# Kernel tuning notes

Measured on AMD Instinct MI355X. Metric: run time of the kernel, lower is better.

## Reference

```python
import jax, jax.numpy as jnp
import numpy as np

N_NODES = 50000
N_EDGES = 800000
IN_CH = 128
HID = 128
OUT_CH = 10
N_GRAPHS = 64
BN_EPS = 1e-5


def _lin_init(k, fan_in, fan_out):
    k1, k2 = jax.random.split(k)
    s = 1.0 / np.sqrt(fan_in)
    W = jax.random.uniform(k1, (fan_in, fan_out), minval=-s, maxval=s, dtype=jnp.float32)
    b = jax.random.uniform(k2, (fan_out,), minval=-s, maxval=s, dtype=jnp.float32)
    return W, b


def setup_inputs() -> dict:
    key = jax.random.key(0)
    ks = jax.random.split(key, 12)
    x = jax.random.normal(ks[0], (N_NODES, IN_CH), dtype=jnp.float32)
    edge_index = jax.random.randint(ks[1], (2, N_EDGES), 0, N_NODES, dtype=jnp.int32)
    batch = jnp.sort(jax.random.randint(ks[2], (N_NODES,), 0, N_GRAPHS, dtype=jnp.int32))
    Wb0, bb0 = _lin_init(ks[3], IN_CH, HID)
    Wb1, bb1 = _lin_init(ks[4], HID, HID)
    Wa0, ba0 = _lin_init(ks[5], HID, HID)
    Wa1, ba1 = _lin_init(ks[6], HID, HID)
    Wa2, ba2 = _lin_init(ks[7], HID, HID)
    Wh0, bh0 = _lin_init(ks[8], HID, HID)
    Wh1, bh1 = _lin_init(ks[9], HID, HID)
    Wh2, bh2 = _lin_init(ks[10], HID, OUT_CH)
    ones = jnp.ones((HID,), jnp.float32)
    zeros = jnp.zeros((HID,), jnp.float32)
    return {
        'x': x, 'edge_index': edge_index, 'batch': batch, 'num_graphs': N_GRAPHS,
        'Wb0': Wb0, 'bb0': bb0, 'gb0': ones, 'betab0': zeros, 'Wb1': Wb1, 'bb1': bb1,
        'Wa0': Wa0, 'ba0': ba0, 'ga0': ones, 'bea0': zeros,
        'Wa1': Wa1, 'ba1': ba1, 'ga1': ones, 'bea1': zeros,
        'Wa2': Wa2, 'ba2': ba2,
        'Wh0': Wh0, 'bh0': bh0, 'Wh1': Wh1, 'bh1': bh1, 'Wh2': Wh2, 'bh2': bh2,
    }


def _gcn_edges(edge_index, n):
    # add self-loops, symmetric deg^{-1/2} normalization (PyG GCNConv default)
    loop = jnp.arange(n, dtype=edge_index.dtype)
    src = jnp.concatenate([edge_index[0], loop])
    dst = jnp.concatenate([edge_index[1], loop])
    deg = jax.ops.segment_sum(jnp.ones_like(dst, dtype=jnp.float32), dst, num_segments=n)
    dinv = jnp.where(deg > 0, jax.lax.rsqrt(deg), 0.0)
    return src, dst, dinv[src] * dinv[dst]


def _conv(h, W, b, src, dst, ew, n):
    hw = h @ W  # [N, F_out]
    agg = jax.ops.segment_sum(hw[src] * ew[:, None], dst, num_segments=n)
    return agg + b


def _bn(h, g, b):
    # BatchNorm1d with track_running_stats=False -> always batch statistics
    mean = jnp.mean(h, axis=0)
    var = jnp.var(h, axis=0)
    return g * (h - mean) * jax.lax.rsqrt(var + BN_EPS) + b


def _gelu(h):
    return jax.nn.gelu(h, approximate=False)


def reference(x, edge_index, batch, num_graphs,
              Wb0, bb0, gb0, betab0, Wb1, bb1,
              Wa0, ba0, ga0, bea0, Wa1, ba1, ga1, bea1, Wa2, ba2,
              Wh0, bh0, Wh1, bh1, Wh2, bh2):
    n = x.shape[0]
    src, dst, ew = _gcn_edges(edge_index, n)
    # GCN stack before (2 layers): conv -> bn -> gelu -> conv
    h = _conv(x, Wb0, bb0, src, dst, ew, n)
    h = _gelu(_bn(h, gb0, betab0))
    h = _conv(h, Wb1, bb1, src, dst, ew, n)
    # GCN stack after (3 layers)
    h = _conv(h, Wa0, ba0, src, dst, ew, n)
    h = _gelu(_bn(h, ga0, bea0))
    h = _conv(h, Wa1, ba1, src, dst, ew, n)
    h = _gelu(_bn(h, ga1, bea1))
    h = _conv(h, Wa2, ba2, src, dst, ew, n)
    # global mean pool per graph
    sums = jax.ops.segment_sum(h, batch, num_segments=num_graphs)
    cnt = jax.ops.segment_sum(jnp.ones((n,), jnp.float32), batch, num_segments=num_graphs)
    pooled = sums / jnp.maximum(cnt, 1.0)[:, None]
    # MLP head (dropout is identity in eval)
    y = _gelu(pooled @ Wh0 + bh0)
    y = _gelu(y @ Wh1 + bh1)
    return y @ Wh2 + bh2
```

## Files before the change

kernel.cpp:

```cpp
#include <hip/hip_runtime.h>
#include <math.h>

#define NN 50000
#define NE 800000
#define CH 128
#define NG 64
#define BN_EPS 1e-5f
#define POOL_CHUNK 64
#define BKT_SHIFT 9
#define NBKT ((NN + 511) >> 9)
#define PTILE 2048

typedef short bfrag8 __attribute__((ext_vector_type(8)));
typedef float facc4 __attribute__((ext_vector_type(4)));

__device__ __forceinline__ float gelu_f(float x) {
    return 0.5f * x * (1.0f + erff(x * 0.70710678118654752440f));
}

__device__ __forceinline__ unsigned int f2bf(float f) {
    unsigned int u = __float_as_uint(f);
    return (u + 0x7FFFu + ((u >> 16) & 1u)) >> 16;
}
__device__ __forceinline__ unsigned int pack_bf2(float lo, float hi) {
    return (f2bf(hi) << 16) | f2bf(lo);
}
__device__ __forceinline__ float bf_lo(unsigned int v) { return __uint_as_float(v << 16); }
__device__ __forceinline__ float bf_hi(unsigned int v) { return __uint_as_float(v & 0xFFFF0000u); }

__global__ __launch_bounds__(256) void bhist_k(const int* __restrict__ ei, int* __restrict__ bcnt) {
    __shared__ int lh[NBKT];
    int t = threadIdx.x;
    int base = blockIdx.x * PTILE;
    if (t < NBKT) lh[t] = 0;
    __syncthreads();
    #pragma unroll
    for (int i = 0; i < 8; ++i) {
        int e = base + i * 256 + t;
        if (e < NE) atomicAdd(&lh[ei[NE + e] >> BKT_SHIFT], 1);
    }
    __syncthreads();
    if (t < NBKT && lh[t]) atomicAdd(&bcnt[t], lh[t]);
}

__global__ __launch_bounds__(128) void bkt_scan_k(const int* __restrict__ bcnt,
                                                  int* __restrict__ boff,
                                                  int* __restrict__ btail,
                                                  int* __restrict__ row_ptr) {
    __shared__ int sh[128];
    int t = threadIdx.x;
    int v = (t < NBKT) ? bcnt[t] : 0;
    sh[t] = v;
    __syncthreads();
    for (int off = 1; off < 128; off <<= 1) {
        int a = (t >= off) ? sh[t - off] : 0;
        __syncthreads();
        sh[t] += a;
        __syncthreads();
    }
    if (t < NBKT) {
        boff[t + 1] = sh[t];
        btail[t] = sh[t] - v;
    }
    if (t == 0) { boff[0] = 0; row_ptr[NN] = NE; }
}

__global__ __launch_bounds__(256) void part_k(const int* __restrict__ ei,
                                              int* __restrict__ btail,
                                              unsigned long long* __restrict__ part) {
    __shared__ int lh[NBKT];
    __shared__ int gbase[NBKT];
    int t = threadIdx.x;
    int base = blockIdx.x * PTILE;
    if (t < NBKT) lh[t] = 0;
    __syncthreads();
    int s[8], d[8], rk[8];
    #pragma unroll
    for (int i = 0; i < 8; ++i) {
        int e = base + i * 256 + t;
        if (e < NE) {
            s[i] = ei[e];
            d[i] = ei[NE + e];
            rk[i] = atomicAdd(&lh[d[i] >> BKT_SHIFT], 1);
        }
    }
    __syncthreads();
    if (t < NBKT && lh[t]) gbase[t] = atomicAdd(&btail[t], lh[t]);
    __syncthreads();
    #pragma unroll
    for (int i = 0; i < 8; ++i) {
        int e = base + i * 256 + t;
        if (e < NE) {
            int b = d[i] >> BKT_SHIFT;
            part[gbase[b] + rk[i]] =
                ((unsigned long long)(unsigned int)d[i] << 32) | (unsigned int)s[i];
        }
    }
}

__global__ __launch_bounds__(256) void cscat2_k(const unsigned long long* __restrict__ part,
                                                const int* __restrict__ boff,
                                                int* __restrict__ row_ptr,
                                                float* __restrict__ dinv,
                                                int* __restrict__ csr_src) {
    __shared__ int cnt_l[512];
    __shared__ int off_l[512];
    __shared__ int psum[256];
    int b = blockIdx.x;
    int n0 = b << BKT_SHIFT;
    int t = threadIdx.x;
    cnt_l[t] = 0;
    cnt_l[t + 256] = 0;
    __syncthreads();
    int e0 = boff[b], e1 = boff[b + 1];
    for (int e = e0 + t; e < e1; e += 256) {
        int d = (int)(part[e] >> 32);
        atomicAdd(&cnt_l[d - n0], 1);
    }
    __syncthreads();
    int c0 = cnt_l[2 * t], c1 = cnt_l[2 * t + 1];
    psum[t] = c0 + c1;
    __syncthreads();
    for (int off = 1; off < 256; off <<= 1) {
        int a = (t >= off) ? psum[t - off] : 0;
        __syncthreads();
        psum[t] += a;
        __syncthreads();
    }
    int excl = (t == 0) ? 0 : psum[t - 1];
    off_l[2 * t] = excl;
    off_l[2 * t + 1] = excl + c0;
    int gbase = boff[b];
    #pragma unroll
    for (int k = 0; k < 2; ++k) {
        int ln = 2 * t + k;
        int n = n0 + ln;
        if (n < NN) {
            int c = (k == 0) ? c0 : c1;
            row_ptr[n] = gbase + off_l[ln];
            dinv[n] = rsqrtf((float)c + 1.0f);
        }
    }
    __syncthreads();
    cnt_l[t] = 0;
    cnt_l[t + 256] = 0;
    __syncthreads();
    for (int e = e0 + t; e < e1; e += 256) {
        unsigned long long p = part[e];
        int s = (int)(unsigned int)p;
        int ld = (int)(p >> 32) - n0;
        int pos = gbase + off_l[ld] + atomicAdd(&cnt_l[ld], 1);
        csr_src[pos] = s;
    }
}

__global__ __launch_bounds__(256) void wconv_k(const float* __restrict__ W,
                                               unsigned short* __restrict__ wf) {
    int u = blockIdx.x * 256 + threadIdx.x;
    int nt = u >> 8, kc = (u >> 6) & 3, l = u & 63;
    int kbase = kc * 32 + (l >> 4) * 8;
    int n = nt * 16 + (l & 15);
    unsigned int p[4];
    #pragma unroll
    for (int jj = 0; jj < 4; ++jj) {
        float a = W[(kbase + 2 * jj) * 128 + n];
        float b = W[(kbase + 2 * jj + 1) * 128 + n];
        p[jj] = pack_bf2(a, b);
    }
    uint4* dst = (uint4*)(wf + (size_t)u * 8);
    *dst = make_uint4(p[0], p[1], p[2], p[3]);
}

__global__ __launch_bounds__(256) void gemm_k(const float* __restrict__ A,
                                              const unsigned short* __restrict__ wfrag,
                                              const float* __restrict__ ss,
                                              unsigned short* __restrict__ out16) {
    __shared__ unsigned short Alds[8192];
    __shared__ unsigned short Wlds[16384];

    const int tid = threadIdx.x;
    const int row0 = blockIdx.x * 64;

    #pragma unroll
    for (int i = 0; i < 4; ++i) {
        int linear = tid + i * 256;
        int r = linear >> 4;
        int g = linear & 15;
        float4 v0 = make_float4(0.f, 0.f, 0.f, 0.f);
        float4 v1 = make_float4(0.f, 0.f, 0.f, 0.f);
        if (row0 + r < NN) {
            const float4* src = (const float4*)&A[(size_t)(row0 + r) * 128 + g * 8];
            v0 = src[0];
            v1 = src[1];
            if (ss) {
                float4 sc0 = ((const float4*)ss)[g * 2];
                float4 sh0 = ((const float4*)ss)[32 + g * 2];
                float4 sc1 = ((const float4*)ss)[g * 2 + 1];
                float4 sh1 = ((const float4*)ss)[32 + g * 2 + 1];
                v0.x = gelu_f(v0.x * sc0.x + sh0.x); v0.y = gelu_f(v0.y * sc0.y + sh0.y);
                v0.z = gelu_f(v0.z * sc0.z + sh0.z); v0.w = gelu_f(v0.w * sc0.w + sh0.w);
                v1.x = gelu_f(v1.x * sc1.x + sh1.x); v1.y = gelu_f(v1.y * sc1.y + sh1.y);
                v1.z = gelu_f(v1.z * sc1.z + sh1.z); v1.w = gelu_f(v1.w * sc1.w + sh1.w);
            }
        }
        int unit = (((r >> 4) * 4 + (g >> 2)) * 64) + ((g & 3) * 16) + (r & 15);
        uint4* dst = (uint4*)(Alds + (size_t)unit * 8);
        *dst = make_uint4(pack_bf2(v0.x, v0.y), pack_bf2(v0.z, v0.w),
                          pack_bf2(v1.x, v1.y), pack_bf2(v1.z, v1.w));
    }
    #pragma unroll
    for (int i = 0; i < 8; ++i) {
        int linear = tid + i * 256;
        ((uint4*)Wlds)[linear] = ((const uint4*)wfrag)[linear];
    }
    __syncthreads();

    const int w = tid >> 6;
    const int l = tid & 63;
    const int quad = l >> 4;
    const int m = l & 15;

    facc4 acc[8];
    #pragma unroll
    for (int nt = 0; nt < 8; ++nt) acc[nt] = (facc4){0.f, 0.f, 0.f, 0.f};

    #pragma unroll
    for (int kc = 0; kc < 4; ++kc) {
        bfrag8 a = *((const bfrag8*)(Alds + ((size_t)((w * 4 + kc) * 64 + l)) * 8));
        #pragma unroll
        for (int nt = 0; nt < 8; ++nt) {
            bfrag8 b = *((const bfrag8*)(Wlds + ((size_t)((nt * 4 + kc) * 64 + l)) * 8));
            acc[nt] = __builtin_amdgcn_mfma_f32_16x16x32_bf16(a, b, acc[nt], 0, 0, 0);
        }
    }

    #pragma unroll
    for (int nt = 0; nt < 8; ++nt) {
        #pragma unroll
        for (int r = 0; r < 4; ++r) {
            int row = row0 + w * 16 + quad * 4 + r;
            if (row < NN) out16[(size_t)row * 128 + nt * 16 + m] = (unsigned short)f2bf(acc[nt][r]);
        }
    }
}

__global__ __launch_bounds__(256) void csr_agg_k(const int* __restrict__ row_ptr,
                                                 const int* __restrict__ csr_src,
                                                 const unsigned int* __restrict__ hw16,
                                                 const float* __restrict__ bias,
                                                 const float* __restrict__ dinv,
                                                 float* __restrict__ out) {
    int node = (blockIdx.x * 256 + threadIdx.x) >> 6;
    if (node >= NN) return;
    int lane = threadIdx.x & 63;

    float di = dinv[node];
    float sw = di * di;
    float2 b = ((const float2*)bias)[lane];
    unsigned int hs = hw16[(size_t)node * 64 + lane];
    float selfx = b.x + bf_lo(hs) * sw;
    float selfy = b.y + bf_hi(hs) * sw;

    float a0x = 0.f, a0y = 0.f, a1x = 0.f, a1y = 0.f;
    float a2x = 0.f, a2y = 0.f, a3x = 0.f, a3y = 0.f;

    int j = row_ptr[node];
    int j1 = row_ptr[node + 1];
    for (; j + 7 < j1; j += 8) {
        int s[8];
        #pragma unroll
        for (int k = 0; k < 8; ++k) s[k] = csr_src[j + k];
        float w[8];
        #pragma unroll
        for (int k = 0; k < 8; ++k) w[k] = dinv[s[k]];
        unsigned int v[8];
        #pragma unroll
        for (int k = 0; k < 8; ++k) v[k] = hw16[(size_t)s[k] * 64 + lane];
        a0x += bf_lo(v[0]) * w[0] + bf_lo(v[1]) * w[1];
        a0y += bf_hi(v[0]) * w[0] + bf_hi(v[1]) * w[1];
        a1x += bf_lo(v[2]) * w[2] + bf_lo(v[3]) * w[3];
        a1y += bf_hi(v[2]) * w[2] + bf_hi(v[3]) * w[3];
        a2x += bf_lo(v[4]) * w[4] + bf_lo(v[5]) * w[5];
        a2y += bf_hi(v[4]) * w[4] + bf_hi(v[5]) * w[5];
        a3x += bf_lo(v[6]) * w[6] + bf_lo(v[7]) * w[7];
        a3y += bf_hi(v[6]) * w[6] + bf_hi(v[7]) * w[7];
    }
    for (; j + 1 < j1; j += 2) {
        int s0 = csr_src[j], s1 = csr_src[j + 1];
        float w0 = dinv[s0], w1 = dinv[s1];
        unsigned int v0 = hw16[(size_t)s0 * 64 + lane];
        unsigned int v1 = hw16[(size_t)s1 * 64 + lane];
        a0x += bf_lo(v0) * w0 + bf_lo(v1) * w1;
        a0y += bf_hi(v0) * w0 + bf_hi(v1) * w1;
    }
    if (j < j1) {
        int s = csr_src[j];
        float w = dinv[s];
        unsigned int v = hw16[(size_t)s * 64 + lane];
        a0x += bf_lo(v) * w;
        a0y += bf_hi(v) * w;
    }
    float ox = selfx + di * ((a0x + a1x) + (a2x + a3x));
    float oy = selfy + di * ((a0y + a1y) + (a2y + a3y));
    ((float2*)out)[(size_t)node * 64 + lane] = make_float2(ox, oy);
}

__global__ __launch_bounds__(256) void bn_stats_k(const float* __restrict__ h, float* __restrict__ sums) {
    int c = threadIdx.x & 127;
    int half = threadIdx.x >> 7;
    int r0 = blockIdx.x * 128 + half;
    float s = 0.f, ss = 0.f;
    #pragma unroll 4
    for (int i = 0; i < 64; ++i) {
        int r = r0 + i * 2;
        if (r < NN) {
            float v = h[(size_t)r * 128 + c];
            s += v; ss += v * v;
        }
    }
    __shared__ float sh_s[128], sh_ss[128];
    if (half == 1) { sh_s[c] = s; sh_ss[c] = ss; }
    __syncthreads();
    if (half == 0) {
        atomicAdd(&sums[c], s + sh_s[c]);
        atomicAdd(&sums[128 + c], ss + sh_ss[c]);
    }
}

__global__ __launch_bounds__(128) void bn_finalize_k(const float* __restrict__ sums,
                                                     const float* __restrict__ g,
                                                     const float* __restrict__ beta,
                                                     float* __restrict__ ss) {
    int c = threadIdx.x;
    float mean = sums[c] * (1.0f / NN);
    float var = sums[128 + c] * (1.0f / NN) - mean * mean;
    float sc = g[c] * rsqrtf(var + BN_EPS);
    ss[c] = sc;
    ss[128 + c] = beta[c] - mean * sc;
}

__global__ __launch_bounds__(128) void pool_sum_k(const float* __restrict__ h,
                                                  const int* __restrict__ batch,
                                                  float* __restrict__ sums) {
    int r0 = blockIdx.x * POOL_CHUNK;
    int r1 = min(r0 + POOL_CHUNK, NN);
    if (r0 >= NN) return;
    int c = threadIdx.x;
    float acc = 0.f;
    int g = batch[r0];
    for (int r = r0; r < r1; ++r) {
        int gr = batch[r];
        if (gr != g) {
            atomicAdd(&sums[g * 128 + c], acc);
            acc = 0.f;
            g = gr;
        }
        acc += h[(size_t)r * 128 + c];
    }
    atomicAdd(&sums[g * 128 + c], acc);
}

__device__ __forceinline__ int lower_bound_dev(const int* __restrict__ a, int n, int key) {
    int lo = 0, hi = n;
    while (lo < hi) {
        int mid = (lo + hi) >> 1;
        if (a[mid] < key) lo = mid + 1; else hi = mid;
    }
    return lo;
}

__global__ __launch_bounds__(128) void pool_div_k(const float* __restrict__ sums,
                                                  const int* __restrict__ batch,
                                                  float* __restrict__ pooled) {
    int g = blockIdx.x;
    int a = lower_bound_dev(batch, NN, g);
    int b = lower_bound_dev(batch, NN, g + 1);
    float inv = 1.0f / fmaxf((float)(b - a), 1.0f);
    int c = threadIdx.x;
    pooled[g * 128 + c] = sums[g * 128 + c] * inv;
}

__global__ __launch_bounds__(128) void head_k(const float* __restrict__ pooled,
                                              const float* __restrict__ W0, const float* __restrict__ b0,
                                              const float* __restrict__ W1, const float* __restrict__ b1,
                                              const float* __restrict__ W2, const float* __restrict__ b2,
                                              float* __restrict__ out) {
    __shared__ float r0[128], r1[128];
    int g = blockIdx.x, t = threadIdx.x;
    r0[t] = pooled[g * 128 + t];
    __syncthreads();
    float acc = b0[t];
    for (int k = 0; k < 128; ++k) acc += r0[k] * W0[k * 128 + t];
    r1[t] = gelu_f(acc);
    __syncthreads();
    acc = b1[t];
    for (int k = 0; k < 128; ++k) acc += r1[k] * W1[k * 128 + t];
    float y = gelu_f(acc);
    __syncthreads();
    r0[t] = y;
    __syncthreads();
    if (t < 10) {
        acc = b2[t];
        for (int k = 0; k < 128; ++k) acc += r0[k] * W2[k * 10 + t];
        out[g * 10 + t] = acc;
    }
}

extern "C" void kernel_launch(void* const* d_in, const int* in_sizes, int n_in,
                              void* d_out, int out_size, void* d_ws, size_t ws_size,
                              hipStream_t stream) {
    const float* x      = (const float*)d_in[0];
    const int*   ei     = (const int*)d_in[1];
    const int*   batch  = (const int*)d_in[2];
    const float* Wb0    = (const float*)d_in[4];
    const float* bb0    = (const float*)d_in[5];
    const float* gb0    = (const float*)d_in[6];
    const float* betab0 = (const float*)d_in[7];
    const float* Wb1    = (const float*)d_in[8];
    const float* bb1    = (const float*)d_in[9];
    const float* Wa0    = (const float*)d_in[10];
    const float* ba0    = (const float*)d_in[11];
    const float* ga0    = (const float*)d_in[12];
    const float* bea0   = (const float*)d_in[13];
    const float* Wa1    = (const float*)d_in[14];
    const float* ba1    = (const float*)d_in[15];
    const float* ga1    = (const float*)d_in[16];
    const float* bea1   = (const float*)d_in[17];
    const float* Wa2    = (const float*)d_in[18];
    const float* ba2    = (const float*)d_in[19];
    const float* Wh0    = (const float*)d_in[20];
    const float* bh0    = (const float*)d_in[21];
    const float* Wh1    = (const float*)d_in[22];
    const float* bh1    = (const float*)d_in[23];
    const float* Wh2    = (const float*)d_in[24];
    const float* bh2    = (const float*)d_in[25];
    float* out = (float*)d_out;

    char* ws = (char*)d_ws;
    unsigned int* hw16 = (unsigned int*)ws;            ws += (size_t)NN * 64 * 4;
    float* bufB    = (float*)ws;                       ws += (size_t)NN * CH * 4;
    float* bufC    = (float*)ws;                       ws += (size_t)NN * CH * 4;
    float* dinv    = (float*)ws;                       ws += (size_t)NN * 4;
    int*   row_ptr = (int*)ws;                         ws += (size_t)(NN + 1) * 4;
    int*   csr_src = (int*)ws;                         ws += (size_t)NE * 4;
    unsigned long long* part = (unsigned long long*)ws; ws += (size_t)NE * 8;
    unsigned short* wf = (unsigned short*)ws;          ws += (size_t)5 * 16384 * 2;
    int*   bcnt    = (int*)ws;                         ws += 128 * 4;
    int*   boff    = (int*)ws;                         ws += 128 * 4;
    int*   btail   = (int*)ws;                         ws += 128 * 4;
    float* bnss    = (float*)ws;                       ws += 256 * 4;
    float* ssbuf   = (float*)ws;                       ws += 256 * 4;
    float* psum    = (float*)ws;                       ws += (size_t)NG * CH * 4;
    float* pooled  = (float*)ws;                       ws += (size_t)NG * CH * 4;

    unsigned short* wfb0 = wf;
    unsigned short* wfb1 = wf + 16384;
    unsigned short* wfa0 = wf + 2 * 16384;
    unsigned short* wfa1 = wf + 3 * 16384;
    unsigned short* wfa2 = wf + 4 * 16384;

    wconv_k<<<8, 256, 0, stream>>>(Wb0, wfb0);
    wconv_k<<<8, 256, 0, stream>>>(Wb1, wfb1);
    wconv_k<<<8, 256, 0, stream>>>(Wa0, wfa0);
    wconv_k<<<8, 256, 0, stream>>>(Wa1, wfa1);
    wconv_k<<<8, 256, 0, stream>>>(Wa2, wfa2);

    hipMemsetAsync(bcnt, 0, 128 * sizeof(int), stream);
    bhist_k<<<(NE + PTILE - 1) / PTILE, 256, 0, stream>>>(ei, bcnt);
    bkt_scan_k<<<1, 128, 0, stream>>>(bcnt, boff, btail, row_ptr);
    part_k<<<(NE + PTILE - 1) / PTILE, 256, 0, stream>>>(ei, btail, part);
    cscat2_k<<<NBKT, 256, 0, stream>>>(part, boff, row_ptr, dinv, csr_src);

    auto conv = [&](const float* in, const unsigned short* wfrag, const float* b,
                    const float* ss, float* o) {
        gemm_k<<<(NN + 63) / 64, 256, 0, stream>>>(in, wfrag, ss, (unsigned short*)hw16);
        csr_agg_k<<<(NN * 64 + 255) / 256, 256, 0, stream>>>(row_ptr, csr_src, hw16, b, dinv, o);
    };
    auto bn_stats = [&](const float* h, const float* g, const float* beta) {
        hipMemsetAsync(bnss, 0, 256 * sizeof(float), stream);
        bn_stats_k<<<(NN + 127) / 128, 256, 0, stream>>>(h, bnss);
        bn_finalize_k<<<1, 128, 0, stream>>>(bnss, g, beta, ssbuf);
    };

    conv(x, wfb0, bb0, nullptr, bufB);
    bn_stats(bufB, gb0, betab0);
    conv(bufB, wfb1, bb1, ssbuf, bufC);
    conv(bufC, wfa0, ba0, nullptr, bufB);
    bn_stats(bufB, ga0, bea0);
    conv(bufB, wfa1, ba1, ssbuf, bufC);
    bn_stats(bufC, ga1, bea1);
    conv(bufC, wfa2, ba2, ssbuf, bufB);

    hipMemsetAsync(psum, 0, NG * CH * sizeof(float), stream);
    pool_sum_k<<<(NN + POOL_CHUNK - 1) / POOL_CHUNK, 128, 0, stream>>>(bufB, batch, psum);
    pool_div_k<<<NG, 128, 0, stream>>>(psum, batch, pooled);
    head_k<<<NG, 128, 0, stream>>>(pooled, Wh0, bh0, Wh1, bh1, Wh2, bh2, out);
}
```

Baseline: 595.4 us.

## Store activations in bf16, drop bucket histogram pass, fuse BN finalize and launches

Intermediate node features are now stored as bf16 instead of fp32, which halves the traffic of aggregation, BN stats, GEMM input and pooling. The bucket histogram and scan kernels are removed in favour of fixed-capacity buckets (CAP per bucket) with per-row counts. BN finalize moves into the stats kernel via a last-block counter, weight conversion becomes one launch, and pool division is folded into the head. The fixed capacity assumes no bucket exceeds 16384 edges, and the extra bf16 rounding of activations lowers precision.

```diff
diff --git a/kernel.cpp b/kernel.cpp
--- a/kernel.cpp
+++ b/kernel.cpp
@@ -10,6 +10,7 @@
 #define BKT_SHIFT 9
 #define NBKT ((NN + 511) >> 9)
 #define PTILE 2048
+#define CAP 16384
 
 typedef short bfrag8 __attribute__((ext_vector_type(8)));
 typedef float facc4 __attribute__((ext_vector_type(4)));
@@ -27,43 +28,6 @@
 }
 __device__ __forceinline__ float bf_lo(unsigned int v) { return __uint_as_float(v << 16); }
 __device__ __forceinline__ float bf_hi(unsigned int v) { return __uint_as_float(v & 0xFFFF0000u); }
-
-__global__ __launch_bounds__(256) void bhist_k(const int* __restrict__ ei, int* __restrict__ bcnt) {
-    __shared__ int lh[NBKT];
-    int t = threadIdx.x;
-    int base = blockIdx.x * PTILE;
-    if (t < NBKT) lh[t] = 0;
-    __syncthreads();
-    #pragma unroll
-    for (int i = 0; i < 8; ++i) {
-        int e = base + i * 256 + t;
-        if (e < NE) atomicAdd(&lh[ei[NE + e] >> BKT_SHIFT], 1);
-    }
-    __syncthreads();
-    if (t < NBKT && lh[t]) atomicAdd(&bcnt[t], lh[t]);
-}
-
-__global__ __launch_bounds__(128) void bkt_scan_k(const int* __restrict__ bcnt,
-                                                  int* __restrict__ boff,
-                                                  int* __restrict__ btail,
-                                                  int* __restrict__ row_ptr) {
-    __shared__ int sh[128];
-    int t = threadIdx.x;
-    int v = (t < NBKT) ? bcnt[t] : 0;
-    sh[t] = v;
-    __syncthreads();
-    for (int off = 1; off < 128; off <<= 1) {
-        int a = (t >= off) ? sh[t - off] : 0;
-        __syncthreads();
-        sh[t] += a;
-        __syncthreads();
-    }
-    if (t < NBKT) {
-        boff[t + 1] = sh[t];
-        btail[t] = sh[t] - v;
-    }
-    if (t == 0) { boff[0] = 0; row_ptr[NN] = NE; }
-}
 
 __global__ __launch_bounds__(256) void part_k(const int* __restrict__ ei,
                                               int* __restrict__ btail,
@@ -85,7 +49,7 @@
         }
     }
     __syncthreads();
-    if (t < NBKT && lh[t]) gbase[t] = atomicAdd(&btail[t], lh[t]);
+    if (t < NBKT && lh[t]) gbase[t] = t * CAP + atomicAdd(&btail[t], lh[t]);
     __syncthreads();
     #pragma unroll
     for (int i = 0; i < 8; ++i) {
@@ -99,45 +63,46 @@
 }
 
 __global__ __launch_bounds__(256) void cscat2_k(const unsigned long long* __restrict__ part,
-                                                const int* __restrict__ boff,
+                                                const int* __restrict__ btail,
                                                 int* __restrict__ row_ptr,
+                                                int* __restrict__ row_cnt,
                                                 float* __restrict__ dinv,
                                                 int* __restrict__ csr_src) {
     __shared__ int cnt_l[512];
     __shared__ int off_l[512];
-    __shared__ int psum[256];
+    __shared__ int psc[256];
     int b = blockIdx.x;
     int n0 = b << BKT_SHIFT;
     int t = threadIdx.x;
     cnt_l[t] = 0;
     cnt_l[t + 256] = 0;
     __syncthreads();
-    int e0 = boff[b], e1 = boff[b + 1];
+    int e0 = b * CAP, e1 = e0 + btail[b];
     for (int e = e0 + t; e < e1; e += 256) {
         int d = (int)(part[e] >> 32);
         atomicAdd(&cnt_l[d - n0], 1);
     }
     __syncthreads();
     int c0 = cnt_l[2 * t], c1 = cnt_l[2 * t + 1];
-    psum[t] = c0 + c1;
+    psc[t] = c0 + c1;
     __syncthreads();
     for (int off = 1; off < 256; off <<= 1) {
-        int a = (t >= off) ? psum[t - off] : 0;
+        int a = (t >= off) ? psc[t - off] : 0;
         __syncthreads();
-        psum[t] += a;
+        psc[t] += a;
         __syncthreads();
     }
-    int excl = (t == 0) ? 0 : psum[t - 1];
+    int excl = (t == 0) ? 0 : psc[t - 1];
     off_l[2 * t] = excl;
     off_l[2 * t + 1] = excl + c0;
-    int gbase = boff[b];
     #pragma unroll
     for (int k = 0; k < 2; ++k) {
         int ln = 2 * t + k;
         int n = n0 + ln;
         if (n < NN) {
             int c = (k == 0) ? c0 : c1;
-            row_ptr[n] = gbase + off_l[ln];
+            row_ptr[n] = e0 + off_l[ln];
+            row_cnt[n] = c;
             dinv[n] = rsqrtf((float)c + 1.0f);
         }
     }
@@ -149,14 +114,22 @@
         unsigned long long p = part[e];
         int s = (int)(unsigned int)p;
         int ld = (int)(p >> 32) - n0;
-        int pos = gbase + off_l[ld] + atomicAdd(&cnt_l[ld], 1);
+        int pos = e0 + off_l[ld] + atomicAdd(&cnt_l[ld], 1);
         csr_src[pos] = s;
     }
 }
 
-__global__ __launch_bounds__(256) void wconv_k(const float* __restrict__ W,
-                                               unsigned short* __restrict__ wf) {
-    int u = blockIdx.x * 256 + threadIdx.x;
+__global__ __launch_bounds__(256) void wconv_all_k(const float* __restrict__ W0,
+                                                   const float* __restrict__ W1,
+                                                   const float* __restrict__ W2,
+                                                   const float* __restrict__ W3,
+                                                   const float* __restrict__ W4,
+                                                   unsigned short* __restrict__ wf) {
+    int which = blockIdx.x >> 3;
+    int u = (blockIdx.x & 7) * 256 + threadIdx.x;
+    const float* W = (which == 0) ? W0 : (which == 1) ? W1 : (which == 2) ? W2
+                   : (which == 3) ? W3 : W4;
+    unsigned short* dst_wf = wf + (size_t)which * 16384;
     int nt = u >> 8, kc = (u >> 6) & 3, l = u & 63;
     int kbase = kc * 32 + (l >> 4) * 8;
     int n = nt * 16 + (l & 15);
@@ -167,20 +140,57 @@
         float b = W[(kbase + 2 * jj + 1) * 128 + n];
         p[jj] = pack_bf2(a, b);
     }
-    uint4* dst = (uint4*)(wf + (size_t)u * 8);
-    *dst = make_uint4(p[0], p[1], p[2], p[3]);
-}
-
-__global__ __launch_bounds__(256) void gemm_k(const float* __restrict__ A,
-                                              const unsigned short* __restrict__ wfrag,
-                                              const float* __restrict__ ss,
-                                              unsigned short* __restrict__ out16) {
+    *(uint4*)(dst_wf + (size_t)u * 8) = make_uint4(p[0], p[1], p[2], p[3]);
+}
+
+__device__ __forceinline__ void gemm_core(unsigned short* Alds, unsigned short* Wlds,
+                                          const unsigned short* wfrag, int tid,
+                                          int row0, unsigned int* out16) {
+    #pragma unroll
+    for (int i = 0; i < 8; ++i) {
+        int linear = tid + i * 256;
+        ((uint4*)Wlds)[linear] = ((const uint4*)wfrag)[linear];
+    }
+    __syncthreads();
+
+    const int w = tid >> 6;
+    const int l = tid & 63;
+    const int quad = l >> 4;
+    const int m = l & 15;
+
+    facc4 acc[8];
+    #pragma unroll
+    for (int nt = 0; nt < 8; ++nt) acc[nt] = (facc4){0.f, 0.f, 0.f, 0.f};
+
+    #pragma unroll
+    for (int kc = 0; kc < 4; ++kc) {
+        bfrag8 a = *((const bfrag8*)(Alds + ((size_t)((w * 4 + kc) * 64 + l)) * 8));
+        #pragma unroll
+        for (int nt = 0; nt < 8; ++nt) {
+            bfrag8 b = *((const bfrag8*)(Wlds + ((size_t)((nt * 4 + kc) * 64 + l)) * 8));
+            acc[nt] = __builtin_amdgcn_mfma_f32_16x16x32_bf16(a, b, acc[nt], 0, 0, 0);
+        }
+    }
+
+    #pragma unroll
+    for (int nt = 0; nt < 8; ++nt) {
+        #pragma unroll
+        for (int r = 0; r < 4; ++r) {
+            int row = row0 + w * 16 + quad * 4 + r;
+            if (row < NN)
+                ((unsigned short*)out16)[(size_t)row * 128 + nt * 16 + m] =
+                    (unsigned short)f2bf(acc[nt][r]);
+        }
+    }
+}
+
+__global__ __launch_bounds__(256) void gemm_f32_k(const float* __restrict__ A,
+                                                  const unsigned short* __restrict__ wfrag,
+                                                  unsigned int* __restrict__ out16) {
     __shared__ unsigned short Alds[8192];
     __shared__ unsigned short Wlds[16384];
-
     const int tid = threadIdx.x;
     const int row0 = blockIdx.x * 64;
-
     #pragma unroll
     for (int i = 0; i < 4; ++i) {
         int linear = tid + i * 256;
@@ -192,64 +202,60 @@
             const float4* src = (const float4*)&A[(size_t)(row0 + r) * 128 + g * 8];
             v0 = src[0];
             v1 = src[1];
-            if (ss) {
-                float4 sc0 = ((const float4*)ss)[g * 2];
-                float4 sh0 = ((const float4*)ss)[32 + g * 2];
-                float4 sc1 = ((const float4*)ss)[g * 2 + 1];
-                float4 sh1 = ((const float4*)ss)[32 + g * 2 + 1];
-                v0.x = gelu_f(v0.x * sc0.x + sh0.x); v0.y = gelu_f(v0.y * sc0.y + sh0.y);
-                v0.z = gelu_f(v0.z * sc0.z + sh0.z); v0.w = gelu_f(v0.w * sc0.w + sh0.w);
-                v1.x = gelu_f(v1.x * sc1.x + sh1.x); v1.y = gelu_f(v1.y * sc1.y + sh1.y);
-                v1.z = gelu_f(v1.z * sc1.z + sh1.z); v1.w = gelu_f(v1.w * sc1.w + sh1.w);
-            }
         }
         int unit = (((r >> 4) * 4 + (g >> 2)) * 64) + ((g & 3) * 16) + (r & 15);
-        uint4* dst = (uint4*)(Alds + (size_t)unit * 8);
-        *dst = make_uint4(pack_bf2(v0.x, v0.y), pack_bf2(v0.z, v0.w),
-                          pack_bf2(v1.x, v1.y), pack_bf2(v1.z, v1.w));
-    }
-    #pragma unroll
-    for (int i = 0; i < 8; ++i) {
+        *(uint4*)(Alds + (size_t)unit * 8) =
+            make_uint4(pack_bf2(v0.x, v0.y), pack_bf2(v0.z, v0.w),
+                       pack_bf2(v1.x, v1.y), pack_bf2(v1.z, v1.w));
+    }
+    gemm_core(Alds, Wlds, wfrag, tid, row0, out16);
+}
+
+__global__ __launch_bounds__(256) void gemm_bf16_k(const unsigned int* __restrict__ h16,
+                                                   const unsigned short* __restrict__ wfrag,
+                                                   const float* __restrict__ ss,
+                                                   unsigned int* __restrict__ out16) {
+    __shared__ unsigned short Alds[8192];
+    __shared__ unsigned short Wlds[16384];
+    const int tid = threadIdx.x;
+    const int row0 = blockIdx.x * 64;
+    #pragma unroll
+    for (int i = 0; i < 4; ++i) {
         int linear = tid + i * 256;
-        ((uint4*)Wlds)[linear] = ((const uint4*)wfrag)[linear];
-    }
-    __syncthreads();
-
-    const int w = tid >> 6;
-    const int l = tid & 63;
-    const int quad = l >> 4;
-    const int m = l & 15;
-
-    facc4 acc[8];
-    #pragma unroll
-    for (int nt = 0; nt < 8; ++nt) acc[nt] = (facc4){0.f, 0.f, 0.f, 0.f};
-
-    #pragma unroll
-    for (int kc = 0; kc < 4; ++kc) {
-        bfrag8 a = *((const bfrag8*)(Alds + ((size_t)((w * 4 + kc) * 64 + l)) * 8));
-        #pragma unroll
-        for (int nt = 0; nt < 8; ++nt) {
-            bfrag8 b = *((const bfrag8*)(Wlds + ((size_t)((nt * 4 + kc) * 64 + l)) * 8));
-            acc[nt] = __builtin_amdgcn_mfma_f32_16x16x32_bf16(a, b, acc[nt], 0, 0, 0);
-        }
-    }
-
-    #pragma unroll
-    for (int nt = 0; nt < 8; ++nt) {
-        #pragma unroll
-        for (int r = 0; r < 4; ++r) {
-            int row = row0 + w * 16 + quad * 4 + r;
-            if (row < NN) out16[(size_t)row * 128 + nt * 16 + m] = (unsigned short)f2bf(acc[nt][r]);
-        }
-    }
+        int r = linear >> 4;
+        int g = linear & 15;
+        uint4 v = make_uint4(0u, 0u, 0u, 0u);
+        if (row0 + r < NN)
+            v = ((const uint4*)h16)[(size_t)(row0 + r) * 16 + g];
+        if (ss) {
+            float4 sc0 = ((const float4*)ss)[g * 2];
+            float4 sh0 = ((const float4*)ss)[32 + g * 2];
+            float4 sc1 = ((const float4*)ss)[g * 2 + 1];
+            float4 sh1 = ((const float4*)ss)[32 + g * 2 + 1];
+            float f0 = gelu_f(bf_lo(v.x) * sc0.x + sh0.x);
+            float f1 = gelu_f(bf_hi(v.x) * sc0.y + sh0.y);
+            float f2 = gelu_f(bf_lo(v.y) * sc0.z + sh0.z);
+            float f3 = gelu_f(bf_hi(v.y) * sc0.w + sh0.w);
+            float f4 = gelu_f(bf_lo(v.z) * sc1.x + sh1.x);
+            float f5 = gelu_f(bf_hi(v.z) * sc1.y + sh1.y);
+            float f6 = gelu_f(bf_lo(v.w) * sc1.z + sh1.z);
+            float f7 = gelu_f(bf_hi(v.w) * sc1.w + sh1.w);
+            v = make_uint4(pack_bf2(f0, f1), pack_bf2(f2, f3),
+                           pack_bf2(f4, f5), pack_bf2(f6, f7));
+        }
+        int unit = (((r >> 4) * 4 + (g >> 2)) * 64) + ((g & 3) * 16) + (r & 15);
+        *(uint4*)(Alds + (size_t)unit * 8) = v;
+    }
+    gemm_core(Alds, Wlds, wfrag, tid, row0, out16);
 }
 
 __global__ __launch_bounds__(256) void csr_agg_k(const int* __restrict__ row_ptr,
+                                                 const int* __restrict__ row_cnt,
                                                  const int* __restrict__ csr_src,
                                                  const unsigned int* __restrict__ hw16,
                                                  const float* __restrict__ bias,
                                                  const float* __restrict__ dinv,
-                                                 float* __restrict__ out) {
+                                                 unsigned int* __restrict__ out16) {
     int node = (blockIdx.x * 256 + threadIdx.x) >> 6;
     if (node >= NN) return;
     int lane = threadIdx.x & 63;
@@ -265,7 +271,7 @@
     float a2x = 0.f, a2y = 0.f, a3x = 0.f, a3y = 0.f;
 
     int j = row_ptr[node];
-    int j1 = row_ptr[node + 1];
+    int j1 = j + row_cnt[node];
     for (; j + 7 < j1; j += 8) {
         int s[8];
         #pragma unroll
@@ -302,50 +308,72 @@
     }
     float ox = selfx + di * ((a0x + a1x) + (a2x + a3x));
     float oy = selfy + di * ((a0y + a1y) + (a2y + a3y));
-    ((float2*)out)[(size_t)node * 64 + lane] = make_float2(ox, oy);
-}
-
-__global__ __launch_bounds__(256) void bn_stats_k(const float* __restrict__ h, float* __restrict__ sums) {
-    int c = threadIdx.x & 127;
-    int half = threadIdx.x >> 7;
-    int r0 = blockIdx.x * 128 + half;
-    float s = 0.f, ss = 0.f;
+    out16[(size_t)node * 64 + lane] = pack_bf2(ox, oy);
+}
+
+__global__ __launch_bounds__(256) void bn_stats_k(const unsigned int* __restrict__ h16,
+                                                  float* __restrict__ sums,
+                                                  int* __restrict__ counter,
+                                                  const float* __restrict__ g,
+                                                  const float* __restrict__ beta,
+                                                  float* __restrict__ ssout) {
+    int t = threadIdx.x;
+    int cp = t & 63;
+    int quad = t >> 6;
+    float s0 = 0.f, q0 = 0.f, s1 = 0.f, q1 = 0.f;
+    int r0 = blockIdx.x * 128 + quad;
     #pragma unroll 4
-    for (int i = 0; i < 64; ++i) {
-        int r = r0 + i * 2;
+    for (int i = 0; i < 32; ++i) {
+        int r = r0 + i * 4;
         if (r < NN) {
-            float v = h[(size_t)r * 128 + c];
-            s += v; ss += v * v;
-        }
-    }
-    __shared__ float sh_s[128], sh_ss[128];
-    if (half == 1) { sh_s[c] = s; sh_ss[c] = ss; }
-    __syncthreads();
-    if (half == 0) {
-        atomicAdd(&sums[c], s + sh_s[c]);
-        atomicAdd(&sums[128 + c], ss + sh_ss[c]);
-    }
-}
-
-__global__ __launch_bounds__(128) void bn_finalize_k(const float* __restrict__ sums,
-                                                     const float* __restrict__ g,
-                                                     const float* __restrict__ beta,
-                                                     float* __restrict__ ss) {
-    int c = threadIdx.x;
-    float mean = sums[c] * (1.0f / NN);
-    float var = sums[128 + c] * (1.0f / NN) - mean * mean;
-    float sc = g[c] * rsqrtf(var + BN_EPS);
-    ss[c] = sc;
-    ss[128 + c] = beta[c] - mean * sc;
-}
-
-__global__ __launch_bounds__(128) void pool_sum_k(const float* __restrict__ h,
+            unsigned int v = h16[(size_t)r * 64 + cp];
+            float f0 = bf_lo(v), f1 = bf_hi(v);
+            s0 += f0; q0 += f0 * f0;
+            s1 += f1; q1 += f1 * f1;
+        }
+    }
+    __shared__ float A0[256], A1[256], A2[256], A3[256];
+    A0[t] = s0; A1[t] = q0; A2[t] = s1; A3[t] = q1;
+    __syncthreads();
+    if (t < 64) {
+        float ts0 = A0[t] + A0[64 + t] + A0[128 + t] + A0[192 + t];
+        float tq0 = A1[t] + A1[64 + t] + A1[128 + t] + A1[192 + t];
+        float ts1 = A2[t] + A2[64 + t] + A2[128 + t] + A2[192 + t];
+        float tq1 = A3[t] + A3[64 + t] + A3[128 + t] + A3[192 + t];
+        atomicAdd(&sums[2 * t], ts0);
+        atomicAdd(&sums[2 * t + 1], ts1);
+        atomicAdd(&sums[128 + 2 * t], tq0);
+        atomicAdd(&sums[129 + 2 * t], tq1);
+    }
+    __threadfence();
+    __syncthreads();
+    __shared__ int isLast;
+    if (t == 0) isLast = (atomicAdd(counter, 1) == (int)gridDim.x - 1);
+    __syncthreads();
+    if (isLast) {
+        if (t < 128) {
+            float sv = atomicAdd(&sums[t], 0.f);
+            float qv = atomicAdd(&sums[128 + t], 0.f);
+            float mean = sv * (1.0f / NN);
+            float var = qv * (1.0f / NN) - mean * mean;
+            float sc = g[t] * rsqrtf(var + BN_EPS);
+            ssout[t] = sc;
+            ssout[128 + t] = beta[t] - mean * sc;
+            sums[t] = 0.f;
+            sums[128 + t] = 0.f;
+        }
+        if (t == 0) *counter = 0;
+    }
+}
+
+__global__ __launch_bounds__(128) void pool_sum_k(const unsigned int* __restrict__ h16,
                                                   const int* __restrict__ batch,
                                                   float* __restrict__ sums) {
     int r0 = blockIdx.x * POOL_CHUNK;
     int r1 = min(r0 + POOL_CHUNK, NN);
     if (r0 >= NN) return;
     int c = threadIdx.x;
+    int cp = c >> 1, hi = c & 1;
     float acc = 0.f;
     int g = batch[r0];
     for (int r = r0; r < r1; ++r) {
@@ -355,7 +383,8 @@
             acc = 0.f;
             g = gr;
         }
-        acc += h[(size_t)r * 128 + c];
+        unsigned int v = h16[(size_t)r * 64 + cp];
+        acc += hi ? bf_hi(v) : bf_lo(v);
     }
     atomicAdd(&sums[g * 128 + c], acc);
 }
@@ -369,25 +398,18 @@
     return lo;
 }
 
-__global__ __launch_bounds__(128) void pool_div_k(const float* __restrict__ sums,
-                                                  const int* __restrict__ batch,
-                                                  float* __restrict__ pooled) {
-    int g = blockIdx.x;
-    int a = lower_bound_dev(batch, NN, g);
-    int b = lower_bound_dev(batch, NN, g + 1);
-    float inv = 1.0f / fmaxf((float)(b - a), 1.0f);
-    int c = threadIdx.x;
-    pooled[g * 128 + c] = sums[g * 128 + c] * inv;
-}
-
-__global__ __launch_bounds__(128) void head_k(const float* __restrict__ pooled,
+__global__ __launch_bounds__(128) void head_k(const float* __restrict__ psum,
+                                              const int* __restrict__ batch,
                                               const float* __restrict__ W0, const float* __restrict__ b0,
                                               const float* __restrict__ W1, const float* __restrict__ b1,
                                               const float* __restrict__ W2, const float* __restrict__ b2,
                                               float* __restrict__ out) {
     __shared__ float r0[128], r1[128];
     int g = blockIdx.x, t = threadIdx.x;
-    r0[t] = pooled[g * 128 + t];
+    int a = lower_bound_dev(batch, NN, g);
+    int b = lower_bound_dev(batch, NN, g + 1);
+    float inv = 1.0f / fmaxf((float)(b - a), 1.0f);
+    r0[t] = psum[g * 128 + t] * inv;
     __syncthreads();
     float acc = b0[t];
     for (int k = 0; k < 128; ++k) acc += r0[k] * W0[k * 128 + t];
@@ -437,21 +459,22 @@
     float* out = (float*)d_out;
 
     char* ws = (char*)d_ws;
-    unsigned int* hw16 = (unsigned int*)ws;            ws += (size_t)NN * 64 * 4;
-    float* bufB    = (float*)ws;                       ws += (size_t)NN * CH * 4;
-    float* bufC    = (float*)ws;                       ws += (size_t)NN * CH * 4;
-    float* dinv    = (float*)ws;                       ws += (size_t)NN * 4;
-    int*   row_ptr = (int*)ws;                         ws += (size_t)(NN + 1) * 4;
-    int*   csr_src = (int*)ws;                         ws += (size_t)NE * 4;
-    unsigned long long* part = (unsigned long long*)ws; ws += (size_t)NE * 8;
-    unsigned short* wf = (unsigned short*)ws;          ws += (size_t)5 * 16384 * 2;
-    int*   bcnt    = (int*)ws;                         ws += 128 * 4;
-    int*   boff    = (int*)ws;                         ws += 128 * 4;
-    int*   btail   = (int*)ws;                         ws += 128 * 4;
-    float* bnss    = (float*)ws;                       ws += 256 * 4;
-    float* ssbuf   = (float*)ws;                       ws += 256 * 4;
-    float* psum    = (float*)ws;                       ws += (size_t)NG * CH * 4;
-    float* pooled  = (float*)ws;                       ws += (size_t)NG * CH * 4;
+    unsigned int* hw16 = (unsigned int*)ws;             ws += (size_t)NN * 64 * 4;
+    unsigned int* hB   = (unsigned int*)ws;             ws += (size_t)NN * 64 * 4;
+    unsigned int* hC   = (unsigned int*)ws;             ws += (size_t)NN * 64 * 4;
+    float* dinv    = (float*)ws;                        ws += (size_t)NN * 4;
+    int*   row_ptr = (int*)ws;                          ws += (size_t)(NN + 4) * 4;
+    int*   row_cnt = (int*)ws;                          ws += (size_t)NN * 4;
+    int*   csr_src = (int*)ws;                          ws += (size_t)NBKT * CAP * 4;
+    unsigned long long* part = (unsigned long long*)ws; ws += (size_t)NBKT * CAP * 8;
+    unsigned short* wf = (unsigned short*)ws;           ws += (size_t)5 * 16384 * 2;
+    float* ssbuf   = (float*)ws;                        ws += 256 * 4;
+    char* zbase = ws;
+    int*   btail   = (int*)ws;                          ws += 128 * 4;
+    float* bnsums  = (float*)ws;                        ws += 256 * 4;
+    int*   bncnt   = (int*)ws;                          ws += 4 * 4;
+    float* psum    = (float*)ws;                        ws += (size_t)NG * CH * 4;
+    size_t zbytes = (size_t)(ws - zbase);
 
     unsigned short* wfb0 = wf;
     unsigned short* wfb1 = wf + 16384;
@@ -459,40 +482,34 @@
     unsigned short* wfa1 = wf + 3 * 16384;
     unsigned short* wfa2 = wf + 4 * 16384;
 
-    wconv_k<<<8, 256, 0, stream>>>(Wb0, wfb0);
-    wconv_k<<<8, 256, 0, stream>>>(Wb1, wfb1);
-    wconv_k<<<8, 256, 0, stream>>>(Wa0, wfa0);
-    wconv_k<<<8, 256, 0, stream>>>(Wa1, wfa1);
-    wconv_k<<<8, 256, 0, stream>>>(Wa2, wfa2);
-
-    hipMemsetAsync(bcnt, 0, 128 * sizeof(int), stream);
-    bhist_k<<<(NE + PTILE - 1) / PTILE, 256, 0, stream>>>(ei, bcnt);
-    bkt_scan_k<<<1, 128, 0, stream>>>(bcnt, boff, btail, row_ptr);
+    hipMemsetAsync(zbase, 0, zbytes, stream);
+    wconv_all_k<<<40, 256, 0, stream>>>(Wb0, Wb1, Wa0, Wa1, Wa2, wf);
+
     part_k<<<(NE + PTILE - 1) / PTILE, 256, 0, stream>>>(ei, btail, part);
-    cscat2_k<<<NBKT, 256, 0, stream>>>(part, boff, row_ptr, dinv, csr_src);
-
-    auto conv = [&](const float* in, const unsigned short* wfrag, const float* b,
-                    const float* ss, float* o) {
-        gemm_k<<<(NN + 63) / 64, 256, 0, stream>>>(in, wfrag, ss, (unsigned short*)hw16);
-        csr_agg_k<<<(NN * 64 + 255) / 256, 256, 0, stream>>>(row_ptr, csr_src, hw16, b, dinv, o);
+    cscat2_k<<<NBKT, 256, 0, stream>>>(part, btail, row_ptr, row_cnt, dinv, csr_src);
+
+    auto agg = [&](const float* b, unsigned int* o) {
+        csr_agg_k<<<(NN * 64 + 255) / 256, 256, 0, stream>>>(row_ptr, row_cnt, csr_src,
+                                                             hw16, b, dinv, o);
     };
-    auto bn_stats = [&](const float* h, const float* g, const float* beta) {
-        hipMemsetAsync(bnss, 0, 256 * sizeof(float), stream);
-        bn_stats_k<<<(NN + 127) / 128, 256, 0, stream>>>(h, bnss);
-        bn_finalize_k<<<1, 128, 0, stream>>>(bnss, g, beta, ssbuf);
+    auto bn_stats = [&](const unsigned int* h, const float* g, const float* beta) {
+        bn_stats_k<<<(NN + 127) / 128, 256, 0, stream>>>(h, bnsums, bncnt, g, beta, ssbuf);
     };
 
-    conv(x, wfb0, bb0, nullptr, bufB);
-    bn_stats(bufB, gb0, betab0);
-    conv(bufB, wfb1, bb1, ssbuf, bufC);
-    conv(bufC, wfa0, ba0, nullptr, bufB);
-    bn_stats(bufB, ga0, bea0);
-    conv(bufB, wfa1, ba1, ssbuf, bufC);
-    bn_stats(bufC, ga1, bea1);
-    conv(bufC, wfa2, ba2, ssbuf, bufB);
-
-    hipMemsetAsync(psum, 0, NG * CH * sizeof(float), stream);
-    pool_sum_k<<<(NN + POOL_CHUNK - 1) / POOL_CHUNK, 128, 0, stream>>>(bufB, batch, psum);
-    pool_div_k<<<NG, 128, 0, stream>>>(psum, batch, pooled);
-    head_k<<<NG, 128, 0, stream>>>(pooled, Wh0, bh0, Wh1, bh1, Wh2, bh2, out);
-}
+    gemm_f32_k<<<(NN + 63) / 64, 256, 0, stream>>>(x, wfb0, hw16);
+    agg(bb0, hB);
+    bn_stats(hB, gb0, betab0);
+    gemm_bf16_k<<<(NN + 63) / 64, 256, 0, stream>>>(hB, wfb1, ssbuf, hw16);
+    agg(bb1, hC);
+    gemm_bf16_k<<<(NN + 63) / 64, 256, 0, stream>>>(hC, wfa0, nullptr, hw16);
+    agg(ba0, hB);
+    bn_stats(hB, ga0, bea0);
+    gemm_bf16_k<<<(NN + 63) / 64, 256, 0, stream>>>(hB, wfa1, ssbuf, hw16);
+    agg(ba1, hC);
+    bn_stats(hC, ga1, bea1);
+    gemm_bf16_k<<<(NN + 63) / 64, 256, 0, stream>>>(hC, wfa2, ssbuf, hw16);
+    agg(ba2, hB);
+
+    pool_sum_k<<<(NN + POOL_CHUNK - 1) / POOL_CHUNK, 128, 0, stream>>>(hB, batch, psum);
+    head_k<<<NG, 128, 0, stream>>>(psum, batch, Wh0, bh0, Wh1, bh1, Wh2, bh2, out);
+}
```

After: 592.4 us. About the same (-0.5%).
